# Kernel optimization log

Hardware: AMD Instinct MI355X
Metric: run time of the kernel (lower is better)

Reference implementation:

```python
import jax, jax.numpy as jnp
import numpy as np


def setup_inputs() -> dict:
    key = jax.random.key(0)
    k1, k2, k3 = jax.random.split(key, 3)
    N, M, H = 32768, 4096, 768
    fact = jax.random.normal(k1, (N, H), dtype=jnp.float32)
    elements_p = jax.random.normal(k2, (M, H), dtype=jnp.float32)
    # kaiming_uniform with a=sqrt(5) on [H,H]: bound = sqrt(6/((1+5)*H)) = 1/sqrt(H)
    bound = 1.0 / np.sqrt(H)
    weights = jax.random.uniform(k3, (H, H), dtype=jnp.float32, minval=-bound, maxval=bound)
    return {"fact": fact, "elements_p": elements_p, "weights": weights}


def reference(fact, elements_p, weights):
    # fact: [N,H], elements_p: [M,H], weights: [H,H]
    fact_Q = jnp.max(fact, axis=0, keepdims=True)                 # [1,H]
    f2e = (fact_Q @ weights) @ elements_p.T                        # [1,M]
    f2e = jax.nn.softmax(f2e, axis=-1)
    elements_p_ = jnp.sum(elements_p * f2e.T, axis=0, keepdims=True)  # [1,H]
    e2f = (fact @ weights) @ elements_p_.T                         # [N,1]
    e2f = jax.nn.softmax(e2f, axis=0)
    fact_ = jnp.sum(fact * e2f, axis=0, keepdims=True)             # [1,H]
    return (fact_, elements_p_)
```

## Files before the change

### kernel.cpp

```cpp
#include <hip/hip_runtime.h>
#include <math.h>


#define H 768
#define H4 192
#define PSTRIDE 772
#define ACC_OFF 4
#define NBLK 256
#define NQ 48
#define BASE 0xAAAAAAAAu

__device__ __forceinline__ float wave_max(float x) {
#pragma unroll
  for (int o = 32; o; o >>= 1) x = fmaxf(x, __shfl_xor(x, o, 64));
  return x;
}
__device__ __forceinline__ float wave_sum(float x) {
#pragma unroll
  for (int o = 32; o; o >>= 1) x += __shfl_xor(x, o, 64);
  return x;
}
__device__ __forceinline__ float4 f4max(float4 a, float4 b) {
  return make_float4(fmaxf(a.x, b.x), fmaxf(a.y, b.y), fmaxf(a.z, b.z), fmaxf(a.w, b.w));
}

struct SMem {
  float4 sacc[8][H4];
  float sred[16];
};

__device__ __forceinline__ void stream_pass(const float4* __restrict__ X4,
                                            const float* __restrict__ wvec,
                                            float* __restrict__ part, int R,
                                            SMem& sm) {
  const int tid = threadIdx.x, lane = tid & 63, wv = tid >> 6;
  float4 wr[3];
#pragma unroll
  for (int j = 0; j < 3; ++j) wr[j] = ((const float4*)wvec)[lane + 64 * j];
  const int nw = NBLK * 8;
  const int gw = blockIdx.x * 8 + wv;
  const int rpw = (R + nw - 1) / nw;
  const int r0 = gw * rpw;
  const int r1 = min(R, r0 + rpw);
  float mrun = -INFINITY, l = 0.f;
  float4 acc[3];
#pragma unroll
  for (int j = 0; j < 3; ++j) acc[j] = make_float4(0.f, 0.f, 0.f, 0.f);
  for (int r = r0; r < r1; ++r) {
    const float4* row = X4 + (size_t)r * H4;
    float4 x[3];
    float s = 0.f;
#pragma unroll
    for (int j = 0; j < 3; ++j) {
      x[j] = row[lane + 64 * j];
      s = fmaf(x[j].x, wr[j].x, s);
      s = fmaf(x[j].y, wr[j].y, s);
      s = fmaf(x[j].z, wr[j].z, s);
      s = fmaf(x[j].w, wr[j].w, s);
    }
    s = wave_sum(s);
    const float mn = fmaxf(mrun, s);
    const float esc = __expf(mrun - mn);
    const float p = __expf(s - mn);
    l = fmaf(l, esc, p);
#pragma unroll
    for (int j = 0; j < 3; ++j) {
      acc[j].x = fmaf(acc[j].x, esc, p * x[j].x);
      acc[j].y = fmaf(acc[j].y, esc, p * x[j].y);
      acc[j].z = fmaf(acc[j].z, esc, p * x[j].z);
      acc[j].w = fmaf(acc[j].w, esc, p * x[j].w);
    }
    mrun = mn;
  }
  if (lane == 0) { sm.sred[wv] = mrun; sm.sred[8 + wv] = l; }
#pragma unroll
  for (int j = 0; j < 3; ++j) sm.sacc[wv][lane + 64 * j] = acc[j];
  __syncthreads();
  if (wv == 0) {
    float gm = -INFINITY;
#pragma unroll
    for (int w2 = 0; w2 < 8; ++w2) gm = fmaxf(gm, sm.sred[w2]);
    float fa[8];
    float L = 0.f;
#pragma unroll
    for (int w2 = 0; w2 < 8; ++w2) {
      const float lw = sm.sred[8 + w2];
      fa[w2] = (lw > 0.f) ? __expf(sm.sred[w2] - gm) : 0.f;
      L = fmaf(fa[w2], lw, L);
    }
    float* pb = part + (size_t)blockIdx.x * PSTRIDE;
#pragma unroll
    for (int j = 0; j < 3; ++j) {
      float4 a = make_float4(0.f, 0.f, 0.f, 0.f);
#pragma unroll
      for (int w2 = 0; w2 < 8; ++w2) {
        const float4 t = sm.sacc[w2][lane + 64 * j];
        a.x = fmaf(fa[w2], t.x, a.x);
        a.y = fmaf(fa[w2], t.y, a.y);
        a.z = fmaf(fa[w2], t.z, a.z);
        a.w = fmaf(fa[w2], t.w, a.w);
      }
      *(float4*)(pb + ACC_OFF + 4 * (lane + 64 * j)) = a;
    }
    if (lane == 0) { pb[0] = gm; pb[1] = L; }
  }
}

__global__ __launch_bounds__(192) void k_colmax_q(const float4* __restrict__ x4,
                                                  const float4* __restrict__ W4,
                                                  float4* __restrict__ pmax4, int N,
                                                  unsigned int* __restrict__ cnts,
                                                  float* __restrict__ q,
                                                  float* __restrict__ v) {
  const int t = threadIdx.x;
  if (blockIdx.x == 0) {
    if (t >= 1 && t < 8) cnts[t] = 0u;
#pragma unroll
    for (int j = 0; j < 4; ++j) { q[t + 192 * j] = 0.f; v[t + 192 * j] = 0.f; }
  }
  {
    const int rpb = (N + NBLK - 1) / NBLK;
    const int n0 = blockIdx.x * rpb;
    const int n1 = min(N, n0 + rpb);
    float4 m = make_float4(-INFINITY, -INFINITY, -INFINITY, -INFINITY);
#pragma unroll 8
    for (int n = n0; n < n1; ++n) m = f4max(m, x4[(size_t)n * H4 + t]);
    pmax4[(size_t)blockIdx.x * H4 + t] = m;
  }
  __shared__ unsigned int s_rank;
  __syncthreads();
  if (t == 0) {
    __threadfence();
    s_rank = atomicAdd(cnts + 0, 1u) - BASE;
  }
  __syncthreads();
  const unsigned int rank = s_rank;
  if (rank < (unsigned)(NBLK - NQ)) return;
  if (t == 0) {
    while (__hip_atomic_load(cnts + 0, __ATOMIC_ACQUIRE, __HIP_MEMORY_SCOPE_AGENT) -
               BASE < (unsigned)NBLK)
      __builtin_amdgcn_s_sleep(32);
  }
  __syncthreads();
  __threadfence();

  const int slice = (int)rank - (NBLK - NQ);
  const int k0 = slice * 16;
  const float* pmax = (const float*)pmax4;
  __shared__ float sA[12][16];
  __shared__ float fQl[16];
  {
    const int col = t & 15;
    const int grp = t >> 4;
    float m = -INFINITY;
    for (int p = grp; p < NBLK; p += 12) m = fmaxf(m, pmax[(size_t)p * H + k0 + col]);
    sA[grp][col] = m;
    __syncthreads();
    if (t < 16) {
      float mm = sA[0][t];
#pragma unroll
      for (int g = 1; g < 12; ++g) mm = fmaxf(mm, sA[g][t]);
      fQl[t] = mm;
    }
    __syncthreads();
  }
  float4 acc = make_float4(0.f, 0.f, 0.f, 0.f);
#pragma unroll 4
  for (int kk = 0; kk < 16; ++kk) {
    const float f = fQl[kk];
    const float4 w = W4[(size_t)(k0 + kk) * H4 + t];
    acc.x = fmaf(f, w.x, acc.x);
    acc.y = fmaf(f, w.y, acc.y);
    acc.z = fmaf(f, w.z, acc.z);
    acc.w = fmaf(f, w.w, acc.w);
  }
  atomicAdd(&q[4 * t + 0], acc.x);
  atomicAdd(&q[4 * t + 1], acc.y);
  atomicAdd(&q[4 * t + 2], acc.z);
  atomicAdd(&q[4 * t + 3], acc.w);
}

__global__ __launch_bounds__(512) void k_ep(const float4* __restrict__ ep4,
                                            const float4* __restrict__ W4,
                                            const float* __restrict__ q,
                                            float* __restrict__ pm, int M,
                                            unsigned int* __restrict__ cnt,
                                            float4* __restrict__ out_ep,
                                            float* __restrict__ v) {
  const int tid = threadIdx.x, lane = tid & 63, wv = tid >> 6;
  __shared__ SMem sm;
  stream_pass(ep4, q, pm, M, sm);

  __shared__ unsigned int s_rank;
  __syncthreads();
  if (tid == 0) {
    __threadfence();
    s_rank = atomicAdd(cnt, 1u);
  }
  __syncthreads();
  const unsigned int rank = s_rank;
  if (rank < (unsigned)(NBLK - 8)) return;
  if (tid == 0) {
    while (__hip_atomic_load(cnt, __ATOMIC_ACQUIRE, __HIP_MEMORY_SCOPE_AGENT) <
           (unsigned)NBLK)
      __builtin_amdgcn_s_sleep(8);
  }
  __syncthreads();
  __threadfence();

  const int S = (int)rank - (NBLK - 8);
  __shared__ float se[NBLK];
  __shared__ float4 sep[24];
  const float* P = pm;
  float m = -INFINITY, Lb = 0.f;
  if (tid < NBLK) {
    m = P[(size_t)tid * PSTRIDE];
    Lb = P[(size_t)tid * PSTRIDE + 1];
  }
  float wm = wave_max(m);
  if (lane == 0) sm.sred[wv] = wm;
  __syncthreads();
  float gm = sm.sred[0];
#pragma unroll
  for (int w2 = 1; w2 < 8; ++w2) gm = fmaxf(gm, sm.sred[w2]);
  const float e = (tid < NBLK && Lb > 0.f) ? __expf(m - gm) : 0.f;
  if (tid < NBLK) se[tid] = e;
  float contrib = wave_sum(e * Lb);
  if (lane == 0) sm.sred[8 + wv] = contrib;
  __syncthreads();
  float Lt = sm.sred[8];
#pragma unroll
  for (int w2 = 1; w2 < 8; ++w2) Lt += sm.sred[8 + w2];
  const float invL = 1.f / Lt;
#pragma unroll
  for (int it = 0; it < 3; ++it) {
    const int cl = it * 8 + wv;
    const int c = S * 24 + cl;
    float4 a = make_float4(0.f, 0.f, 0.f, 0.f);
    for (int b = lane; b < NBLK; b += 64) {
      const float eb = se[b];
      const float4 t4 = *(const float4*)(P + (size_t)b * PSTRIDE + ACC_OFF + 4 * c);
      a.x = fmaf(eb, t4.x, a.x);
      a.y = fmaf(eb, t4.y, a.y);
      a.z = fmaf(eb, t4.z, a.z);
      a.w = fmaf(eb, t4.w, a.w);
    }
    a.x = wave_sum(a.x); a.y = wave_sum(a.y);
    a.z = wave_sum(a.z); a.w = wave_sum(a.w);
    if (lane == 0) {
      const float4 r = make_float4(a.x * invL, a.y * invL, a.z * invL, a.w * invL);
      out_ep[c] = r;
      sep[cl] = r;
    }
  }
  __syncthreads();
  float4 er[24];
#pragma unroll
  for (int cl = 0; cl < 24; ++cl) er[cl] = sep[cl];
  for (int i = tid; i < H; i += 512) {
    const float4* wrow = W4 + (size_t)i * H4 + S * 24;
    float s = 0.f;
#pragma unroll
    for (int cl = 0; cl < 24; ++cl) {
      const float4 w = wrow[cl];
      s = fmaf(w.x, er[cl].x, s);
      s = fmaf(w.y, er[cl].y, s);
      s = fmaf(w.z, er[cl].z, s);
      s = fmaf(w.w, er[cl].w, s);
    }
    atomicAdd(&v[i], s);
  }
}

__global__ __launch_bounds__(512) void k_fact(const float4* __restrict__ X4,
                                              const float* __restrict__ v,
                                              float* __restrict__ pn,
                                              float* __restrict__ pn2, int R,
                                              unsigned int* __restrict__ cntA,
                                              unsigned int* __restrict__ cntB,
                                              float* __restrict__ outp) {
  const int tid = threadIdx.x, lane = tid & 63, wv = tid >> 6;
  __shared__ SMem sm;
  stream_pass(X4, v, pn, R, sm);

  __shared__ unsigned int s_rank;
  __syncthreads();
  if (tid == 0) {
    __threadfence();
    s_rank = atomicAdd(cntA, 1u);
  }
  __syncthreads();
  const unsigned int rank = s_rank;
  if (rank < (unsigned)(NBLK - 8)) return;
  if (tid == 0) {
    while (__hip_atomic_load(cntA, __ATOMIC_ACQUIRE, __HIP_MEMORY_SCOPE_AGENT) <
           (unsigned)NBLK)
      __builtin_amdgcn_s_sleep(8);
  }
  __syncthreads();
  __threadfence();

  const int slice = (int)rank - (NBLK - 8);
  const float* Pb = pn + (size_t)slice * 32 * PSTRIDE;
  __shared__ float s32m[32], s32l[32];
  if (tid < 32) {
    s32m[tid] = Pb[(size_t)tid * PSTRIDE];
    s32l[tid] = Pb[(size_t)tid * PSTRIDE + 1];
  }
  __syncthreads();
  float gms = -INFINITY;
#pragma unroll
  for (int b = 0; b < 32; ++b) gms = fmaxf(gms, s32m[b]);
  float4 a[3];
#pragma unroll
  for (int j = 0; j < 3; ++j) a[j] = make_float4(0.f, 0.f, 0.f, 0.f);
  for (int b = wv; b < 32; b += 8) {
    const float e = (s32l[b] > 0.f) ? __expf(s32m[b] - gms) : 0.f;
    const float4* pa = (const float4*)(Pb + (size_t)b * PSTRIDE + ACC_OFF);
#pragma unroll
    for (int j = 0; j < 3; ++j) {
      const float4 t = pa[lane + 64 * j];
      a[j].x = fmaf(e, t.x, a[j].x);
      a[j].y = fmaf(e, t.y, a[j].y);
      a[j].z = fmaf(e, t.z, a[j].z);
      a[j].w = fmaf(e, t.w, a[j].w);
    }
  }
  float lc = 0.f;
  if (tid < 32) lc = ((s32l[tid] > 0.f) ? __expf(s32m[tid] - gms) : 0.f) * s32l[tid];
  lc = wave_sum(lc);
  __syncthreads();
#pragma unroll
  for (int j = 0; j < 3; ++j) sm.sacc[wv][lane + 64 * j] = a[j];
  if (tid == 0) sm.sred[0] = lc;
  __syncthreads();
  float* qb = pn2 + (size_t)slice * PSTRIDE;
  if (tid < H4) {
    float4 s = sm.sacc[0][tid];
#pragma unroll
    for (int w2 = 1; w2 < 8; ++w2) {
      const float4 t = sm.sacc[w2][tid];
      s.x += t.x; s.y += t.y; s.z += t.z; s.w += t.w;
    }
    *(float4*)(qb + ACC_OFF + 4 * tid) = s;
  }
  if (tid == 0) { qb[0] = gms; qb[1] = sm.sred[0]; }

  __syncthreads();
  __shared__ unsigned int s_r2;
  if (tid == 0) {
    __threadfence();
    s_r2 = atomicAdd(cntB, 1u);
  }
  __syncthreads();
  if (s_r2 != 7u) return;
  __threadfence();

  __shared__ float s8m[8], s8l[8];
  if (tid < 8) {
    s8m[tid] = pn2[(size_t)tid * PSTRIDE];
    s8l[tid] = pn2[(size_t)tid * PSTRIDE + 1];
  }
  __syncthreads();
  float gm = -INFINITY;
#pragma unroll
  for (int k = 0; k < 8; ++k) gm = fmaxf(gm, s8m[k]);
  float Lt = 0.f;
#pragma unroll
  for (int k = 0; k < 8; ++k)
    Lt += ((s8l[k] > 0.f) ? __expf(s8m[k] - gm) : 0.f) * s8l[k];
  float4 b[3];
  {
    const int k = wv;
    const float e = (s8l[k] > 0.f) ? __expf(s8m[k] - gm) : 0.f;
    const float4* pa = (const float4*)(pn2 + (size_t)k * PSTRIDE + ACC_OFF);
#pragma unroll
    for (int j = 0; j < 3; ++j) {
      const float4 t = pa[lane + 64 * j];
      b[j] = make_float4(e * t.x, e * t.y, e * t.z, e * t.w);
    }
  }
  __syncthreads();
#pragma unroll
  for (int j = 0; j < 3; ++j) sm.sacc[wv][lane + 64 * j] = b[j];
  __syncthreads();
  if (tid < H4) {
    float4 s = sm.sacc[0][tid];
#pragma unroll
    for (int w2 = 1; w2 < 8; ++w2) {
      const float4 t = sm.sacc[w2][tid];
      s.x += t.x; s.y += t.y; s.z += t.z; s.w += t.w;
    }
    const float inv = 1.f / Lt;
    ((float4*)outp)[tid] = make_float4(s.x * inv, s.y * inv, s.z * inv, s.w * inv);
  }
}

extern "C" void kernel_launch(void* const* d_in, const int* in_sizes, int n_in,
                              void* d_out, int out_size, void* d_ws, size_t ws_size,
                              hipStream_t stream) {
  const float4* fact4 = (const float4*)d_in[0];
  const float4* ep4   = (const float4*)d_in[1];
  const float4* W4    = (const float4*)d_in[2];
  float* out = (float*)d_out;
  const int N = in_sizes[0] / H;
  const int M = in_sizes[1] / H;

  float* wsf = (float*)d_ws;
  unsigned int* cnts = (unsigned int*)d_ws;
  float* q     = wsf + 8;
  float* v     = wsf + 776;
  float* pmaxf = wsf + 1544;
  float* pm    = wsf + 198152;
  float* pn    = wsf + 395784;
  float* pn2   = wsf + 593416;

  k_colmax_q<<<NBLK, 192, 0, stream>>>(fact4, W4, (float4*)pmaxf, N, cnts, q, v);
  k_ep<<<NBLK, 512, 0, stream>>>(ep4, W4, q, pm, M, cnts + 1,
                                 (float4*)(out + H), v);
  k_fact<<<NBLK, 512, 0, stream>>>(fact4, v, pn, pn2, N, cnts + 2, cnts + 3, out);
}
```

Before: 253.5 us.

## Split streaming softmax pass into two interleaved chains and widen colmax blocks

The streaming online-softmax pass now processes two independent halves of each wave's rows together, so two row loads are in flight and two dependent reduction/exp chains overlap, and the partial results are merged at the end. The column-max kernel goes from 192 to 768 threads per block, splitting rows four ways and reducing through shared memory, and the q projection is split the same way. Both changes aim to raise memory-level parallelism in bandwidth-bound streaming. The cost is more registers per thread, which may reduce occupancy, plus an extra shared-memory reduction step.

```diff
diff --git a/kernel.cpp b/kernel.cpp
--- a/kernel.cpp
+++ b/kernel.cpp
@@ -29,10 +29,10 @@
   float sred[16];
 };
 
-__device__ __forceinline__ void stream_pass(const float4* __restrict__ X4,
-                                            const float* __restrict__ wvec,
-                                            float* __restrict__ part, int R,
-                                            SMem& sm) {
+__device__ __forceinline__ void stream_pass2(const float4* __restrict__ X4,
+                                             const float* __restrict__ wvec,
+                                             float* __restrict__ part, int R,
+                                             SMem& sm) {
   const int tid = threadIdx.x, lane = tid & 63, wv = tid >> 6;
   float4 wr[3];
 #pragma unroll
@@ -42,36 +42,80 @@
   const int rpw = (R + nw - 1) / nw;
   const int r0 = gw * rpw;
   const int r1 = min(R, r0 + rpw);
-  float mrun = -INFINITY, l = 0.f;
+  const int cnt = max(r1 - r0, 0);
+  const int half = (cnt + 1) >> 1;
+  float mA = -INFINITY, lA = 0.f, mB = -INFINITY, lB = 0.f;
+  float4 aA[3], aB[3];
+#pragma unroll
+  for (int j = 0; j < 3; ++j) {
+    aA[j] = make_float4(0.f, 0.f, 0.f, 0.f);
+    aB[j] = make_float4(0.f, 0.f, 0.f, 0.f);
+  }
+  for (int i = 0; i < half; ++i) {
+    const int rA = r0 + i;
+    const int rBr = r0 + half + i;
+    const bool bv = rBr < r1;
+    const int rB = bv ? rBr : r0;
+    const float4* rowA = X4 + (size_t)rA * H4;
+    const float4* rowB = X4 + (size_t)rB * H4;
+    float4 xA[3], xB[3];
+    float sA = 0.f, sB = 0.f;
+#pragma unroll
+    for (int j = 0; j < 3; ++j) {
+      xA[j] = rowA[lane + 64 * j];
+      xB[j] = rowB[lane + 64 * j];
+    }
+#pragma unroll
+    for (int j = 0; j < 3; ++j) {
+      sA = fmaf(xA[j].x, wr[j].x, sA); sB = fmaf(xB[j].x, wr[j].x, sB);
+      sA = fmaf(xA[j].y, wr[j].y, sA); sB = fmaf(xB[j].y, wr[j].y, sB);
+      sA = fmaf(xA[j].z, wr[j].z, sA); sB = fmaf(xB[j].z, wr[j].z, sB);
+      sA = fmaf(xA[j].w, wr[j].w, sA); sB = fmaf(xB[j].w, wr[j].w, sB);
+    }
+#pragma unroll
+    for (int o = 32; o; o >>= 1) {
+      sA += __shfl_xor(sA, o, 64);
+      sB += __shfl_xor(sB, o, 64);
+    }
+    {
+      const float mn = fmaxf(mA, sA);
+      const float esc = __expf(mA - mn);
+      const float p = __expf(sA - mn);
+      lA = fmaf(lA, esc, p);
+#pragma unroll
+      for (int j = 0; j < 3; ++j) {
+        aA[j].x = fmaf(aA[j].x, esc, p * xA[j].x);
+        aA[j].y = fmaf(aA[j].y, esc, p * xA[j].y);
+        aA[j].z = fmaf(aA[j].z, esc, p * xA[j].z);
+        aA[j].w = fmaf(aA[j].w, esc, p * xA[j].w);
+      }
+      mA = mn;
+    }
+    if (bv) {
+      const float mn = fmaxf(mB, sB);
+      const float esc = __expf(mB - mn);
+      const float p = __expf(sB - mn);
+      lB = fmaf(lB, esc, p);
+#pragma unroll
+      for (int j = 0; j < 3; ++j) {
+        aB[j].x = fmaf(aB[j].x, esc, p * xB[j].x);
+        aB[j].y = fmaf(aB[j].y, esc, p * xB[j].y);
+        aB[j].z = fmaf(aB[j].z, esc, p * xB[j].z);
+        aB[j].w = fmaf(aB[j].w, esc, p * xB[j].w);
+      }
+      mB = mn;
+    }
+  }
+  const float mrun = fmaxf(mA, mB);
+  const float eA = (lA > 0.f) ? __expf(mA - mrun) : 0.f;
+  const float eB = (lB > 0.f) ? __expf(mB - mrun) : 0.f;
+  const float l = eA * lA + eB * lB;
   float4 acc[3];
 #pragma unroll
-  for (int j = 0; j < 3; ++j) acc[j] = make_float4(0.f, 0.f, 0.f, 0.f);
-  for (int r = r0; r < r1; ++r) {
-    const float4* row = X4 + (size_t)r * H4;
-    float4 x[3];
-    float s = 0.f;
-#pragma unroll
-    for (int j = 0; j < 3; ++j) {
-      x[j] = row[lane + 64 * j];
-      s = fmaf(x[j].x, wr[j].x, s);
-      s = fmaf(x[j].y, wr[j].y, s);
-      s = fmaf(x[j].z, wr[j].z, s);
-      s = fmaf(x[j].w, wr[j].w, s);
-    }
-    s = wave_sum(s);
-    const float mn = fmaxf(mrun, s);
-    const float esc = __expf(mrun - mn);
-    const float p = __expf(s - mn);
-    l = fmaf(l, esc, p);
-#pragma unroll
-    for (int j = 0; j < 3; ++j) {
-      acc[j].x = fmaf(acc[j].x, esc, p * x[j].x);
-      acc[j].y = fmaf(acc[j].y, esc, p * x[j].y);
-      acc[j].z = fmaf(acc[j].z, esc, p * x[j].z);
-      acc[j].w = fmaf(acc[j].w, esc, p * x[j].w);
-    }
-    mrun = mn;
-  }
+  for (int j = 0; j < 3; ++j)
+    acc[j] = make_float4(eA * aA[j].x + eB * aB[j].x, eA * aA[j].y + eB * aB[j].y,
+                         eA * aA[j].z + eB * aB[j].z, eA * aA[j].w + eB * aB[j].w);
+
   if (lane == 0) { sm.sred[wv] = mrun; sm.sred[8 + wv] = l; }
 #pragma unroll
   for (int j = 0; j < 3; ++j) sm.sacc[wv][lane + 64 * j] = acc[j];
@@ -106,26 +150,37 @@
   }
 }
 
-__global__ __launch_bounds__(192) void k_colmax_q(const float4* __restrict__ x4,
+__global__ __launch_bounds__(768) void k_colmax_q(const float4* __restrict__ x4,
                                                   const float4* __restrict__ W4,
                                                   float4* __restrict__ pmax4, int N,
                                                   unsigned int* __restrict__ cnts,
                                                   float* __restrict__ q,
                                                   float* __restrict__ v) {
   const int t = threadIdx.x;
+  const int col = t % H4;
+  const int rs = t / H4;
+  __shared__ float4 smax[4][H4];
+  __shared__ float sA[48][16];
+  __shared__ float fQl[16];
   if (blockIdx.x == 0) {
     if (t >= 1 && t < 8) cnts[t] = 0u;
-#pragma unroll
-    for (int j = 0; j < 4; ++j) { q[t + 192 * j] = 0.f; v[t + 192 * j] = 0.f; }
+    if (t < H4) {
+#pragma unroll
+      for (int j = 0; j < 4; ++j) { q[t + H4 * j] = 0.f; v[t + H4 * j] = 0.f; }
+    }
   }
   {
     const int rpb = (N + NBLK - 1) / NBLK;
-    const int n0 = blockIdx.x * rpb;
-    const int n1 = min(N, n0 + rpb);
+    const int nbase = blockIdx.x * rpb;
+    const int n1 = min(N, nbase + rpb);
     float4 m = make_float4(-INFINITY, -INFINITY, -INFINITY, -INFINITY);
 #pragma unroll 8
-    for (int n = n0; n < n1; ++n) m = f4max(m, x4[(size_t)n * H4 + t]);
-    pmax4[(size_t)blockIdx.x * H4 + t] = m;
+    for (int n = nbase + rs; n < n1; n += 4) m = f4max(m, x4[(size_t)n * H4 + col]);
+    smax[rs][col] = m;
+    __syncthreads();
+    if (t < H4)
+      pmax4[(size_t)blockIdx.x * H4 + t] =
+          f4max(f4max(smax[0][t], smax[1][t]), f4max(smax[2][t], smax[3][t]));
   }
   __shared__ unsigned int s_rank;
   __syncthreads();
@@ -139,7 +194,7 @@
   if (t == 0) {
     while (__hip_atomic_load(cnts + 0, __ATOMIC_ACQUIRE, __HIP_MEMORY_SCOPE_AGENT) -
                BASE < (unsigned)NBLK)
-      __builtin_amdgcn_s_sleep(32);
+      __builtin_amdgcn_s_sleep(16);
   }
   __syncthreads();
   __threadfence();
@@ -147,37 +202,42 @@
   const int slice = (int)rank - (NBLK - NQ);
   const int k0 = slice * 16;
   const float* pmax = (const float*)pmax4;
-  __shared__ float sA[12][16];
-  __shared__ float fQl[16];
   {
-    const int col = t & 15;
+    const int colq = t & 15;
     const int grp = t >> 4;
     float m = -INFINITY;
-    for (int p = grp; p < NBLK; p += 12) m = fmaxf(m, pmax[(size_t)p * H + k0 + col]);
-    sA[grp][col] = m;
+    for (int p = grp; p < NBLK; p += 48) m = fmaxf(m, pmax[(size_t)p * H + k0 + colq]);
+    sA[grp][colq] = m;
     __syncthreads();
     if (t < 16) {
       float mm = sA[0][t];
 #pragma unroll
-      for (int g = 1; g < 12; ++g) mm = fmaxf(mm, sA[g][t]);
+      for (int g = 1; g < 48; ++g) mm = fmaxf(mm, sA[g][t]);
       fQl[t] = mm;
     }
     __syncthreads();
   }
-  float4 acc = make_float4(0.f, 0.f, 0.f, 0.f);
-#pragma unroll 4
-  for (int kk = 0; kk < 16; ++kk) {
-    const float f = fQl[kk];
-    const float4 w = W4[(size_t)(k0 + kk) * H4 + t];
-    acc.x = fmaf(f, w.x, acc.x);
-    acc.y = fmaf(f, w.y, acc.y);
-    acc.z = fmaf(f, w.z, acc.z);
-    acc.w = fmaf(f, w.w, acc.w);
-  }
-  atomicAdd(&q[4 * t + 0], acc.x);
-  atomicAdd(&q[4 * t + 1], acc.y);
-  atomicAdd(&q[4 * t + 2], acc.z);
-  atomicAdd(&q[4 * t + 3], acc.w);
+  {
+    float4 acc = make_float4(0.f, 0.f, 0.f, 0.f);
+#pragma unroll
+    for (int kk = 4 * rs; kk < 4 * rs + 4; ++kk) {
+      const float f = fQl[kk];
+      const float4 w = W4[(size_t)(k0 + kk) * H4 + col];
+      acc.x = fmaf(f, w.x, acc.x);
+      acc.y = fmaf(f, w.y, acc.y);
+      acc.z = fmaf(f, w.z, acc.z);
+      acc.w = fmaf(f, w.w, acc.w);
+    }
+    smax[rs][col] = acc;
+    __syncthreads();
+    if (t < H4) {
+      const float4 a0 = smax[0][t], a1 = smax[1][t], a2 = smax[2][t], a3 = smax[3][t];
+      atomicAdd(&q[4 * t + 0], a0.x + a1.x + a2.x + a3.x);
+      atomicAdd(&q[4 * t + 1], a0.y + a1.y + a2.y + a3.y);
+      atomicAdd(&q[4 * t + 2], a0.z + a1.z + a2.z + a3.z);
+      atomicAdd(&q[4 * t + 3], a0.w + a1.w + a2.w + a3.w);
+    }
+  }
 }
 
 __global__ __launch_bounds__(512) void k_ep(const float4* __restrict__ ep4,
@@ -189,7 +249,7 @@
                                             float* __restrict__ v) {
   const int tid = threadIdx.x, lane = tid & 63, wv = tid >> 6;
   __shared__ SMem sm;
-  stream_pass(ep4, q, pm, M, sm);
+  stream_pass2(ep4, q, pm, M, sm);
 
   __shared__ unsigned int s_rank;
   __syncthreads();
@@ -281,7 +341,7 @@
                                               float* __restrict__ outp) {
   const int tid = threadIdx.x, lane = tid & 63, wv = tid >> 6;
   __shared__ SMem sm;
-  stream_pass(X4, v, pn, R, sm);
+  stream_pass2(X4, v, pn, R, sm);
 
   __shared__ unsigned int s_rank;
   __syncthreads();
@@ -415,7 +475,7 @@
   float* pn    = wsf + 395784;
   float* pn2   = wsf + 593416;
 
-  k_colmax_q<<<NBLK, 192, 0, stream>>>(fact4, W4, (float4*)pmaxf, N, cnts, q, v);
+  k_colmax_q<<<NBLK, 768, 0, stream>>>(fact4, W4, (float4*)pmaxf, N, cnts, q, v);
   k_ep<<<NBLK, 512, 0, stream>>>(ep4, W4, q, pm, M, cnts + 1,
                                  (float4*)(out + H), v);
   k_fact<<<NBLK, 512, 0, stream>>>(fact4, v, pn, pn2, N, cnts + 2, cnts + 3, out);
```

Result: slower. 272.3 us (+7.4%).
